# Performance work log

Hardware: AMD Instinct MI355X
Metric: run time of the kernel (lower is better)

The kernel has to match this reference:

```python
import jax, jax.numpy as jnp
import numpy as np

N_NODES = 50000
N_EDGES = 600000
D_EMB = 128
D_HID = 128
N_HEADS = 4
N_MABS = 7  # ISAB0(mab0,mab1), ISAB1(mab0,mab1), PMA, SAB, SAB
B, S = 16, 512
PROTO = 5


def setup_inputs() -> dict:
    key = jax.random.key(0)
    ks = jax.random.split(key, 24)
    nrm = lambda k, shape, s=0.05: jax.random.normal(k, shape, jnp.float32) * s
    node_embed = nrm(ks[0], (N_NODES + 1, D_EMB), 1.0).at[0].set(0.0)  # padding_idx=0
    return {
        'node_ids': jax.random.randint(ks[1], (B, S), 0, N_NODES),
        'edge_idx': jax.random.randint(ks[2], (2, N_EDGES), 0, N_NODES),
        'edge_attr': jax.random.normal(ks[3], (N_EDGES,), jnp.float32),
        'node_embed': node_embed,
        'lin_W': nrm(ks[4], (D_EMB, D_HID)), 'lin_b': jnp.zeros((D_HID,), jnp.float32),
        'gat_W': nrm(ks[5], (D_HID, D_HID)),
        'gat_att_src': nrm(ks[6], (D_HID,)), 'gat_att_dst': nrm(ks[7], (D_HID,)),
        'gat_bias': jnp.zeros((D_HID,), jnp.float32),
        'mab_Wq': nrm(ks[8], (N_MABS, D_HID, D_HID)), 'mab_bq': jnp.zeros((N_MABS, D_HID), jnp.float32),
        'mab_Wk': nrm(ks[9], (N_MABS, D_HID, D_HID)), 'mab_bk': jnp.zeros((N_MABS, D_HID), jnp.float32),
        'mab_Wv': nrm(ks[10], (N_MABS, D_HID, D_HID)), 'mab_bv': jnp.zeros((N_MABS, D_HID), jnp.float32),
        'mab_Wo': nrm(ks[11], (N_MABS, D_HID, D_HID)), 'mab_bo': jnp.zeros((N_MABS, D_HID), jnp.float32),
        'isab_I': nrm(ks[12], (2, 1, D_HID), 1.0),   # 2 ISAB blocks, num_inds=1
        'pma_S': nrm(ks[13], (1, D_HID), 1.0),       # num_outputs=1 seed
        'dec_W': nrm(ks[14], (D_HID, D_HID)), 'dec_b': jnp.zeros((D_HID,), jnp.float32),
        'prototypes': nrm(ks[15], (1, PROTO, D_HID), 1.0),
    }


def mab(Q, K, Wq, bq, Wk, bk, Wv, bv, Wo, bo):
    # Set-transformer MAB, ln=False; residual uses projected Q; scale by sqrt(full dim)
    D = Q.shape[-1]
    h, d = N_HEADS, D // N_HEADS
    Qp = Q @ Wq + bq
    Kp = K @ Wk + bk
    Vp = K @ Wv + bv
    sh = lambda x: x.reshape(x.shape[0], x.shape[1], h, d).transpose(0, 2, 1, 3)
    A = jax.nn.softmax(jnp.einsum('bhqd,bhkd->bhqk', sh(Qp), sh(Kp)) / np.sqrt(D).astype(np.float32))
    O = sh(Qp) + jnp.einsum('bhqk,bhkd->bhqd', A, sh(Vp))
    O = O.transpose(0, 2, 1, 3).reshape(Q.shape[0], Q.shape[1], D)
    return O + jax.nn.relu(O @ Wo + bo)


def reference(node_ids, edge_idx, edge_attr, node_embed, lin_W, lin_b, gat_W,
              gat_att_src, gat_att_dst, gat_bias, mab_Wq, mab_bq, mab_Wk, mab_bk,
              mab_Wv, mab_bv, mab_Wo, mab_bo, isab_I, pma_S, dec_W, dec_b, prototypes):
    # embed all nodes then linear
    x = node_embed[jnp.arange(N_NODES)] @ lin_W + lin_b          # [N, H]
    # GATConv (1 head, negative_slope=0.2, add_self_loops=True; edge_attr unused)
    loops = jnp.arange(N_NODES)
    src = jnp.concatenate([edge_idx[0], loops])
    dst = jnp.concatenate([edge_idx[1], loops])
    xw = x @ gat_W                                               # [N, H]
    a_s = xw @ gat_att_src                                       # [N]
    a_d = xw @ gat_att_dst
    e = jax.nn.leaky_relu(a_s[src] + a_d[dst], 0.2)              # [E+N]
    m = jax.ops.segment_max(e, dst, num_segments=N_NODES)
    ex = jnp.exp(e - m[dst])
    den = jax.ops.segment_sum(ex, dst, num_segments=N_NODES)
    coef = ex / den[dst]
    x = jax.ops.segment_sum(coef[:, None] * xw[src], dst, num_segments=N_NODES) + gat_bias
    # gather per-sample node sets
    X = x[node_ids]                                              # [B, S, H]
    b = X.shape[0]
    def mb(i, Q, K):
        return mab(Q, K, mab_Wq[i], mab_bq[i], mab_Wk[i], mab_bk[i],
                   mab_Wv[i], mab_bv[i], mab_Wo[i], mab_bo[i])
    # encoder: 2 ISAB blocks (num_inds=1)
    for i in range(2):
        Hb = mb(2 * i, jnp.broadcast_to(isab_I[i][None], (b, 1, D_HID)), X)
        X = mb(2 * i + 1, X, Hb)
    # decoder: PMA -> SAB -> SAB -> Linear
    X = mb(4, jnp.broadcast_to(pma_S[None], (b, 1, D_HID)), X)
    X = mb(5, X, X)
    X = mb(6, X, X)
    X = X @ dec_W + dec_b                                        # [B, 1, H]
    proto = jnp.broadcast_to(prototypes, (b, PROTO, D_HID))
    return jnp.concatenate([X, proto], axis=1)                   # [B, 6, H]
```

## Files before the change

kernel.cpp:

```cpp
#include <hip/hip_runtime.h>
#include <math.h>

#define N_NODES 50000
#define N_EDGES 600000
#define BATCH 16
#define SEQ 512
#define NROWS (BATCH*SEQ)
#define N_ITEMS (N_EDGES + N_NODES)

#define OFF_X      0L
#define OFF_ACC    1048576L
#define OFF_X2     2097152L
#define OFF_AS     3145728L
#define OFF_AD     3195728L
#define OFF_WC     3245728L
#define OFF_BC     3262112L
#define OFF_QP     3262240L
#define OFF_WKH    3262624L
#define OFF_CKH    3264160L
#define OFF_VAS    3264176L
#define OFF_VAD    3264304L
#define OFF_BFIN   3264432L
#define OFF_CSD    3264560L
#define OFF_VPOD   3264564L
#define OFF_PWH    3266612L
#define OFF_PWL    3307572L
#define OFF_MASK   3348532L
#define OFF_DEG    (OFF_MASK + 50000L)
#define OFF_FILL   (OFF_DEG + 8192L)
#define OFF_CNT    (OFF_FILL + 8192L)
#define ZERO_BYTES ((50000L + 8192L + 8192L + 4L) * 4L)
#define OFF_MAP    (OFF_CNT + 4L)
#define OFF_INV    (OFF_MAP + 50000L)
#define OFF_ROWPTR (OFF_INV + 8192L)
#define OFF_COL    (OFF_ROWPTR + 8194L)

typedef __attribute__((ext_vector_type(8))) short bf16x8;
typedef __attribute__((ext_vector_type(4))) float f32x4;
#define MFMA16(a,b,c) __builtin_amdgcn_mfma_f32_16x16x32_bf16(a,b,c,0,0,0)

__device__ __forceinline__ unsigned short f2bf_rne(float f) {
    unsigned int u = __float_as_uint(f);
    unsigned int r = u + 0x7FFFu + ((u >> 16) & 1u);
    return (unsigned short)(r >> 16);
}
__device__ __forceinline__ float bf2f(unsigned short h) {
    return __uint_as_float(((unsigned int)h) << 16);
}

__global__ __launch_bounds__(256) void prep_kernel(
    const float* __restrict__ lin_W, const float* __restrict__ lin_b,
    const float* __restrict__ gat_W,
    const float* __restrict__ mab_Wq, const float* __restrict__ mab_bq,
    const float* __restrict__ isab_I, const float* __restrict__ pma_S,
    float* __restrict__ Wc, float* __restrict__ bc, float* __restrict__ qp)
{
    int t = blockIdx.x * 256 + threadIdx.x;
    if (t < 16384) {
        int i = t >> 7, j = t & 127;
        float s = 0.f;
        for (int k = 0; k < 128; ++k) s += lin_W[i*128 + k] * gat_W[k*128 + j];
        Wc[t] = s;
    } else if (t < 16512) {
        int j = t - 16384;
        float s = 0.f;
        for (int k = 0; k < 128; ++k) s += lin_b[k] * gat_W[k*128 + j];
        bc[j] = s;
    } else if (t < 16896) {
        int u = t - 16512;
        int m = u >> 7, c = u & 127;
        int mi = m * 2;
        const float* vec = (m == 0) ? isab_I : (m == 1 ? isab_I + 128 : pma_S);
        float s = mab_bq[mi*128 + c];
        for (int k = 0; k < 128; ++k) s += vec[k] * mab_Wq[mi*16384 + k*128 + c];
        qp[u] = s;
    }
}

__global__ __launch_bounds__(256) void pack2_kernel(
    const float* __restrict__ Wc, const float* __restrict__ bc,
    const float* __restrict__ qp,
    const float* __restrict__ mab_Wq, const float* __restrict__ mab_Wo,
    const float* __restrict__ mab_Wk, const float* __restrict__ mab_bk,
    const float* __restrict__ att_src, const float* __restrict__ att_dst,
    const float* __restrict__ gat_bias,
    unsigned short* __restrict__ pWh, unsigned short* __restrict__ pWl,
    float* __restrict__ wkh, float* __restrict__ ckh,
    float* __restrict__ vas, float* __restrict__ vad,
    float* __restrict__ bfin, float* __restrict__ csd)
{
    int b = blockIdx.x, t = threadIdx.x;
    if (b < 320) {
        int tid = b*256 + t;
        int m = tid >> 14;
        int e = tid & 16383;
        int j = e & 7, l = (e>>3) & 63, ct = (e>>9) & 7, kc = e >> 12;
        int k = kc*32 + (l>>4)*8 + j;
        int c = ct*16 + (l & 15);
        const float* src;
        if (m == 0) src = Wc;
        else if (m == 1) src = mab_Wq + 1*16384;
        else if (m == 2) src = mab_Wo + 1*16384;
        else if (m == 3) src = mab_Wq + 3*16384;
        else src = mab_Wo + 3*16384;
        float v = src[k*128 + c];
        unsigned short h = f2bf_rne(v);
        pWh[tid] = h;
        pWl[tid] = f2bf_rne(v - bf2f(h));
    } else if (b == 320) {
        for (int it = 0; it < 6; ++it) {
            int u = it*256 + t;
            int m = u >> 9, h = (u >> 7) & 3, j = u & 127;
            const float* Wk = mab_Wk + (2*m)*16384 + j*128 + h*32;
            const float* q  = qp + m*128 + h*32;
            float s = 0.f;
            #pragma unroll
            for (int d = 0; d < 32; ++d) s += Wk[d] * q[d];
            wkh[u] = s;
        }
        if (t < 12) {
            int m = t >> 2, h = t & 3;
            const float* bk = mab_bk + (2*m)*128 + h*32;
            const float* q  = qp + m*128 + h*32;
            float s = 0.f;
            #pragma unroll
            for (int d = 0; d < 32; ++d) s += bk[d] * q[d];
            ckh[t] = s;
        }
    } else {
        if (t < 128) {
            float s = 0.f;
            for (int j = 0; j < 128; ++j) s += Wc[t*128 + j] * att_src[j];
            vas[t] = s;
            bfin[t] = bc[t] + gat_bias[t];
        } else {
            int k = t - 128;
            float s = 0.f;
            for (int j = 0; j < 128; ++j) s += Wc[k*128 + j] * att_dst[j];
            vad[k] = s;
        }
        if (t == 0) {
            float s = 0.f;
            for (int j = 0; j < 128; ++j) s += bc[j] * att_src[j];
            csd[0] = s;
        }
        if (t == 1) {
            float s = 0.f;
            for (int j = 0; j < 128; ++j) s += bc[j] * att_dst[j];
            csd[1] = s;
        }
    }
}

__device__ __forceinline__ void mfma_stage(
    const float (*Xs)[132], int arow, int ao, int lane,
    const unsigned short* __restrict__ pWh, const unsigned short* __restrict__ pWl,
    f32x4 acc[8])
{
    #pragma unroll
    for (int kc = 0; kc < 4; ++kc) {
        float4 fa = *(const float4*)&Xs[arow][kc*32 + ao];
        float4 fb = *(const float4*)&Xs[arow][kc*32 + ao + 4];
        float f[8] = {fa.x, fa.y, fa.z, fa.w, fb.x, fb.y, fb.z, fb.w};
        bf16x8 ah, al;
        #pragma unroll
        for (int j = 0; j < 8; ++j) {
            unsigned short h = f2bf_rne(f[j]);
            ah[j] = (short)h;
            al[j] = (short)f2bf_rne(f[j] - bf2f(h));
        }
        #pragma unroll
        for (int ct = 0; ct < 8; ++ct) {
            int fo = ((kc*8 + ct)*64 + lane)*8;
            bf16x8 bh = *(const bf16x8*)(pWh + fo);
            bf16x8 bl = *(const bf16x8*)(pWl + fo);
            acc[ct] = MFMA16(ah, bh, acc[ct]);
            acc[ct] = MFMA16(ah, bl, acc[ct]);
            acc[ct] = MFMA16(al, bh, acc[ct]);
        }
    }
}

__global__ __launch_bounds__(256) void mfma_lin_kernel(
    const float* __restrict__ Xin,
    const unsigned short* __restrict__ pWh, const unsigned short* __restrict__ pWl,
    const float* __restrict__ b1, float* __restrict__ out)
{
    __shared__ float Xs[64][132];
    int t = threadIdx.x;
    long row0 = (long)blockIdx.x * 64;
    #pragma unroll
    for (int i = 0; i < 32; ++i) {
        int idx = i*256 + t;
        int r = idx >> 7, k = idx & 127;
        Xs[r][k] = Xin[(row0 + r)*128 + k];
    }
    __syncthreads();
    int lane = t & 63, wv = t >> 6;
    int arow = wv*16 + (lane & 15), ao = (lane >> 4)*8;
    int crow0 = wv*16 + (lane >> 4)*4, ccol = lane & 15;
    f32x4 acc[8];
    #pragma unroll
    for (int ct = 0; ct < 8; ++ct) { acc[ct][0]=0.f; acc[ct][1]=0.f; acc[ct][2]=0.f; acc[ct][3]=0.f; }
    mfma_stage(Xs, arow, ao, lane, pWh, pWl, acc);
    #pragma unroll
    for (int ct = 0; ct < 8; ++ct) {
        int cc = ct*16 + ccol;
        float bb = b1[cc];
        #pragma unroll
        for (int i = 0; i < 4; ++i)
            out[(row0 + crow0 + i)*128 + cc] = acc[ct][i] + bb;
    }
}

__global__ __launch_bounds__(256) void mfma_odd_kernel(
    const float* __restrict__ Xin,
    const unsigned short* __restrict__ pQh, const unsigned short* __restrict__ pQl,
    const float* __restrict__ bq, const float* __restrict__ vpod,
    const unsigned short* __restrict__ pOh, const unsigned short* __restrict__ pOl,
    const float* __restrict__ bo, float* __restrict__ Xout)
{
    __shared__ float Xs[64][132];
    int t = threadIdx.x;
    long row0 = (long)blockIdx.x * 64;
    #pragma unroll
    for (int i = 0; i < 32; ++i) {
        int idx = i*256 + t;
        int r = idx >> 7, k = idx & 127;
        Xs[r][k] = Xin[(row0 + r)*128 + k];
    }
    __syncthreads();
    int lane = t & 63, wv = t >> 6;
    int arow = wv*16 + (lane & 15), ao = (lane >> 4)*8;
    int crow0 = wv*16 + (lane >> 4)*4, ccol = lane & 15;
    int bidx = (int)(row0 >> 9);
    f32x4 acc[8];
    #pragma unroll
    for (int ct = 0; ct < 8; ++ct) { acc[ct][0]=0.f; acc[ct][1]=0.f; acc[ct][2]=0.f; acc[ct][3]=0.f; }
    mfma_stage(Xs, arow, ao, lane, pQh, pQl, acc);
    #pragma unroll
    for (int ct = 0; ct < 8; ++ct) {
        int cc = ct*16 + ccol;
        float bb = bq[cc] + vpod[bidx*128 + cc];
        #pragma unroll
        for (int i = 0; i < 4; ++i) Xs[crow0 + i][cc] = acc[ct][i] + bb;
    }
    #pragma unroll
    for (int ct = 0; ct < 8; ++ct) { acc[ct][0]=0.f; acc[ct][1]=0.f; acc[ct][2]=0.f; acc[ct][3]=0.f; }
    mfma_stage(Xs, arow, ao, lane, pOh, pOl, acc);
    #pragma unroll
    for (int ct = 0; ct < 8; ++ct) {
        int cc = ct*16 + ccol;
        float bb = bo[cc];
        #pragma unroll
        for (int i = 0; i < 4; ++i) {
            float o1 = Xs[crow0 + i][cc];
            Xout[(row0 + crow0 + i)*128 + cc] = o1 + fmaxf(acc[ct][i] + bb, 0.f);
        }
    }
}

__global__ __launch_bounds__(256) void avec_kernel(
    const float* __restrict__ embed, const float* __restrict__ vas,
    const float* __restrict__ vad, const float* __restrict__ csd,
    const int* __restrict__ node_ids, int* __restrict__ mask,
    float* __restrict__ a_s, float* __restrict__ a_d)
{
    if (blockIdx.x < 32) {
        int idx = blockIdx.x*256 + threadIdx.x;
        mask[node_ids[idx]] = 1;
    }
    int w = threadIdx.x >> 6, lane = threadIdx.x & 63;
    long row = (long)blockIdx.x * 4 + w;
    const float* xr = embed + row*128 + lane*2;
    float x0 = xr[0], x1 = xr[1];
    float s = x0*vas[lane*2] + x1*vas[lane*2 + 1];
    float d = x0*vad[lane*2] + x1*vad[lane*2 + 1];
    #pragma unroll
    for (int off = 32; off > 0; off >>= 1) {
        s += __shfl_down(s, off);
        d += __shfl_down(d, off);
    }
    if (lane == 0) { a_s[row] = s + csd[0]; a_d[row] = d + csd[1]; }
}

__global__ __launch_bounds__(256) void assign_kernel(
    const int* __restrict__ mask, int* __restrict__ map,
    int* __restrict__ inv, int* __restrict__ counter)
{
    __shared__ int wbase[4];
    int i = blockIdx.x*256 + threadIdx.x;
    bool act = (i < N_NODES) && mask[i];
    unsigned long long m = __ballot(act);
    int lane = threadIdx.x & 63;
    int w = threadIdx.x >> 6;
    if (lane == 0) wbase[w] = __popcll(m);
    __syncthreads();
    if (threadIdx.x == 0) {
        int tot = wbase[0] + wbase[1] + wbase[2] + wbase[3];
        int base = atomicAdd(counter, tot);
        int r = base;
        #pragma unroll
        for (int j = 0; j < 4; ++j) { int cj = wbase[j]; wbase[j] = r; r += cj; }
    }
    __syncthreads();
    if (i < N_NODES) {
        int c = -1;
        if (act) {
            c = wbase[w] + __popcll(m & ((1ull << lane) - 1ull));
            inv[c] = i;
        }
        map[i] = c;
    }
}

__global__ __launch_bounds__(256) void pass1_kernel(
    const int* __restrict__ edge_idx, const int* __restrict__ map,
    int* __restrict__ deg)
{
    int i = blockIdx.x*256 + threadIdx.x;
    if (i >= N_ITEMS) return;
    int dd = (i < N_EDGES) ? edge_idx[N_EDGES + i] : i - N_EDGES;
    int c = map[dd];
    if (c >= 0) atomicAdd(&deg[c], 1);
}

__global__ __launch_bounds__(256) void scan_kernel(const int* __restrict__ deg,
                                                   int* __restrict__ rowptr)
{
    __shared__ int part[256];
    __shared__ int pref[256];
    int t = threadIdx.x;
    int base = t * 32;
    int s = 0;
    #pragma unroll
    for (int j = 0; j < 32; ++j) s += deg[base + j];
    part[t] = s;
    __syncthreads();
    if (t == 0) {
        int run = 0;
        for (int i = 0; i < 256; ++i) { pref[i] = run; run += part[i]; }
    }
    __syncthreads();
    int run = pref[t];
    #pragma unroll
    for (int j = 0; j < 32; ++j) { rowptr[base + j] = run; run += deg[base + j]; }
    if (t == 255) rowptr[8192] = run;
}

__global__ __launch_bounds__(256) void pass2_kernel(
    const int* __restrict__ edge_idx, const int* __restrict__ map,
    const int* __restrict__ rowptr, int* __restrict__ fill,
    int* __restrict__ colx)
{
    int i = blockIdx.x*256 + threadIdx.x;
    if (i >= N_ITEMS) return;
    int s, dd;
    if (i < N_EDGES) { s = edge_idx[i]; dd = edge_idx[N_EDGES + i]; }
    else             { s = dd = i - N_EDGES; }
    int c = map[dd];
    if (c < 0) return;
    int pos = rowptr[c] + atomicAdd(&fill[c], 1);
    colx[pos] = s;
}

__global__ __launch_bounds__(256) void agg_kernel(
    const int* __restrict__ rowptr, const int* __restrict__ colx,
    const int* __restrict__ inv, const int* __restrict__ cnt,
    const float* __restrict__ a_s, const float* __restrict__ a_d,
    const float* __restrict__ embed, float* __restrict__ acc)
{
    int c = blockIdx.x*4 + (threadIdx.x >> 6);
    int lane = threadIdx.x & 63;
    if (c >= *cnt) return;
    int dd = inv[c];
    float ad = a_d[dd];
    int beg = rowptr[c], end = rowptr[c + 1];
    float s0 = 0.f, s1 = 0.f, den = 0.f;
    for (int j = beg; j < end; ++j) {
        int s = colx[j];
        float e = a_s[s] + ad;
        e = (e > 0.f) ? e : 0.2f * e;
        float ex = __expf(e);
        den += ex;
        float2 v = *(const float2*)(embed + (long)s*128 + lane*2);
        s0 += ex * v.x;
        s1 += ex * v.y;
    }
    float inv_d = 1.f / den;
    float* o = acc + (long)c*128 + lane*2;
    o[0] = s0 * inv_d;
    o[1] = s1 * inv_d;
}

__global__ __launch_bounds__(256) void gather_kernel(
    const int* __restrict__ node_ids, const int* __restrict__ map,
    const float* __restrict__ X2, float* __restrict__ X)
{
    int w = threadIdx.x >> 6, lane = threadIdx.x & 63;
    int j = blockIdx.x*4 + w;
    int c = map[node_ids[j]];
    const float2 v = *(const float2*)(X2 + (long)c*128 + lane*2);
    *(float2*)(X + (long)j*128 + lane*2) = v;
}

__device__ __forceinline__ float matvec_qs(
    const float* __restrict__ W, const float* xs, float (*red)[128], int t)
{
    int c = t & 127, q = t >> 7;
    float acc = 0.f;
    #pragma unroll
    for (int j = 0; j < 32; ++j) {
        int k = q*32 + j;
        acc += xs[k] * W[k*128 + c];
    }
    red[q][c] = acc;
    __syncthreads();
    float s = 0.f;
    if (t < 128) s = red[0][t] + red[1][t] + red[2][t] + red[3][t];
    __syncthreads();
    return s;
}

__global__ __launch_bounds__(512) void attn_even_kernel(
    const float* __restrict__ X, const float* __restrict__ qp,
    const float* __restrict__ wkh, const float* __restrict__ ckh,
    const float* __restrict__ Wv, const float* __restrict__ bv,
    const float* __restrict__ Wo, const float* __restrict__ bo,
    const float* __restrict__ Wv1, const float* __restrict__ bv1,
    float* __restrict__ vpod)
{
    __shared__ float l_sm[4][512];
    __shared__ float part[4][4][128];
    __shared__ float wks[4][128];
    __shared__ float u_sm[4][128];
    __shared__ float red[4][128];
    __shared__ float red64[4][64];
    __shared__ float mx[4], dn[4];
    __shared__ float qs[128], Ovec[128], Hsm[128];
    int b = blockIdx.x, t = threadIdx.x;
    if (t < 128) qs[t] = qp[t];
    wks[t >> 7][t & 127] = wkh[t];
    __syncthreads();
    const float scale = 0.088388347648318447f;
    float ck0 = ckh[0], ck1 = ckh[1], ck2 = ckh[2], ck3 = ckh[3];
    {
        const float* xr = X + ((long)b*512 + t)*128;
        float l[4] = {0.f, 0.f, 0.f, 0.f};
        for (int d4 = 0; d4 < 128; d4 += 4) {
            float4 xv = *(const float4*)&xr[d4];
            #pragma unroll
            for (int h = 0; h < 4; ++h)
                l[h] += xv.x*wks[h][d4] + xv.y*wks[h][d4+1]
                      + xv.z*wks[h][d4+2] + xv.w*wks[h][d4+3];
        }
        l_sm[0][t] = (l[0] + ck0) * scale;
        l_sm[1][t] = (l[1] + ck1) * scale;
        l_sm[2][t] = (l[2] + ck2) * scale;
        l_sm[3][t] = (l[3] + ck3) * scale;
    }
    __syncthreads();
    if (t < 256) {
        int h = t >> 6, i = t & 63;
        float m = -1e30f;
        #pragma unroll
        for (int j = 0; j < 8; ++j) m = fmaxf(m, l_sm[h][i + 64*j]);
        red64[h][i] = m;
    }
    __syncthreads();
    if (t < 4) {
        float m = -1e30f;
        for (int i = 0; i < 64; ++i) m = fmaxf(m, red64[t][i]);
        mx[t] = m;
    }
    __syncthreads();
    #pragma unroll
    for (int h = 0; h < 4; ++h) l_sm[h][t] = __expf(l_sm[h][t] - mx[h]);
    __syncthreads();
    if (t < 256) {
        int h = t >> 6, i = t & 63;
        float ssum = 0.f;
        #pragma unroll
        for (int j = 0; j < 8; ++j) ssum += l_sm[h][i + 64*j];
        red64[h][i] = ssum;
    }
    __syncthreads();
    if (t < 4) {
        float sm = 0.f;
        for (int i = 0; i < 64; ++i) sm += red64[t][i];
        dn[t] = 1.f / sm;
    }
    __syncthreads();
    {
        int q4 = t >> 7, d = t & 127;
        float a0 = 0.f, a1 = 0.f, a2 = 0.f, a3 = 0.f;
        const float* xc = X + ((long)b*512 + q4*128)*128 + d;
        for (int kk = 0; kk < 128; ++kk) {
            float xv = xc[(long)kk*128];
            int k = q4*128 + kk;
            a0 += xv * l_sm[0][k];
            a1 += xv * l_sm[1][k];
            a2 += xv * l_sm[2][k];
            a3 += xv * l_sm[3][k];
        }
        part[q4][0][d] = a0; part[q4][1][d] = a1; part[q4][2][d] = a2; part[q4][3][d] = a3;
    }
    __syncthreads();
    {
        int h = t >> 7, d = t & 127;
        u_sm[h][d] = (part[0][h][d] + part[1][h][d] + part[2][h][d] + part[3][h][d]) * dn[h];
    }
    __syncthreads();
    {
        int q4 = t >> 7, c = t & 127, h = c >> 5;
        float a = 0.f;
        #pragma unroll
        for (int j = 0; j < 32; ++j) {
            int k = q4*32 + j;
            a += u_sm[h][k] * Wv[k*128 + c];
        }
        red[q4][c] = a;
    }
    __syncthreads();
    if (t < 128) Ovec[t] = qs[t] + red[0][t] + red[1][t] + red[2][t] + red[3][t] + bv[t];
    __syncthreads();
    float mv = matvec_qs(Wo, Ovec, red, t);
    if (t < 128) Hsm[t] = Ovec[t] + fmaxf(mv + bo[t], 0.f);
    __syncthreads();
    float mv2 = matvec_qs(Wv1, Hsm, red, t);
    if (t < 128) vpod[b*128 + t] = mv2 + bv1[t];
}

__global__ __launch_bounds__(512) void attn_pma_kernel(
    const float* __restrict__ X, const float* __restrict__ qp,
    const float* __restrict__ wkh, const float* __restrict__ ckh,
    const float* __restrict__ mab_Wq, const float* __restrict__ mab_bq,
    const float* __restrict__ mab_Wv, const float* __restrict__ mab_bv,
    const float* __restrict__ mab_Wo, const float* __restrict__ mab_bo,
    const float* __restrict__ dec_W, const float* __restrict__ dec_b,
    const float* __restrict__ protos, float* __restrict__ out)
{
    __shared__ float l_sm[4][512];
    __shared__ float part[4][4][128];
    __shared__ float wks[4][128];
    __shared__ float u_sm[4][128];
    __shared__ float red[4][128];
    __shared__ float red64[4][64];
    __shared__ float mx[4], dn[4];
    __shared__ float qs[128], Ovec[128], S1[128], S2[128];
    int b = blockIdx.x, t = threadIdx.x;
    if (t < 128) qs[t] = qp[t];
    wks[t >> 7][t & 127] = wkh[t];
    __syncthreads();
    const float scale = 0.088388347648318447f;
    float ck0 = ckh[0], ck1 = ckh[1], ck2 = ckh[2], ck3 = ckh[3];
    {
        const float* xr = X + ((long)b*512 + t)*128;
        float l[4] = {0.f, 0.f, 0.f, 0.f};
        for (int d4 = 0; d4 < 128; d4 += 4) {
            float4 xv = *(const float4*)&xr[d4];
            #pragma unroll
            for (int h = 0; h < 4; ++h)
                l[h] += xv.x*wks[h][d4] + xv.y*wks[h][d4+1]
                      + xv.z*wks[h][d4+2] + xv.w*wks[h][d4+3];
        }
        l_sm[0][t] = (l[0] + ck0) * scale;
        l_sm[1][t] = (l[1] + ck1) * scale;
        l_sm[2][t] = (l[2] + ck2) * scale;
        l_sm[3][t] = (l[3] + ck3) * scale;
    }
    __syncthreads();
    if (t < 256) {
        int h = t >> 6, i = t & 63;
        float m = -1e30f;
        #pragma unroll
        for (int j = 0; j < 8; ++j) m = fmaxf(m, l_sm[h][i + 64*j]);
        red64[h][i] = m;
    }
    __syncthreads();
    if (t < 4) {
        float m = -1e30f;
        for (int i = 0; i < 64; ++i) m = fmaxf(m, red64[t][i]);
        mx[t] = m;
    }
    __syncthreads();
    #pragma unroll
    for (int h = 0; h < 4; ++h) l_sm[h][t] = __expf(l_sm[h][t] - mx[h]);
    __syncthreads();
    if (t < 256) {
        int h = t >> 6, i = t & 63;
        float ssum = 0.f;
        #pragma unroll
        for (int j = 0; j < 8; ++j) ssum += l_sm[h][i + 64*j];
        red64[h][i] = ssum;
    }
    __syncthreads();
    if (t < 4) {
        float sm = 0.f;
        for (int i = 0; i < 64; ++i) sm += red64[t][i];
        dn[t] = 1.f / sm;
    }
    __syncthreads();
    {
        int q4 = t >> 7, d = t & 127;
        float a0 = 0.f, a1 = 0.f, a2 = 0.f, a3 = 0.f;
        const float* xc = X + ((long)b*512 + q4*128)*128 + d;
        for (int kk = 0; kk < 128; ++kk) {
            float xv = xc[(long)kk*128];
            int k = q4*128 + kk;
            a0 += xv * l_sm[0][k];
            a1 += xv * l_sm[1][k];
            a2 += xv * l_sm[2][k];
            a3 += xv * l_sm[3][k];
        }
        part[q4][0][d] = a0; part[q4][1][d] = a1; part[q4][2][d] = a2; part[q4][3][d] = a3;
    }
    __syncthreads();
    {
        int h = t >> 7, d = t & 127;
        u_sm[h][d] = (part[0][h][d] + part[1][h][d] + part[2][h][d] + part[3][h][d]) * dn[h];
    }
    __syncthreads();
    {
        int q4 = t >> 7, c = t & 127, h = c >> 5;
        float a = 0.f;
        #pragma unroll
        for (int j = 0; j < 32; ++j) {
            int k = q4*32 + j;
            a += u_sm[h][k] * (mab_Wv + 4*16384)[k*128 + c];
        }
        red[q4][c] = a;
    }
    __syncthreads();
    if (t < 128) Ovec[t] = qs[t] + red[0][t] + red[1][t] + red[2][t] + red[3][t]
                         + mab_bv[4*128 + t];
    __syncthreads();
    float mv = matvec_qs(mab_Wo + 4*16384, Ovec, red, t);
    if (t < 128) S1[t] = Ovec[t] + fmaxf(mv + mab_bo[4*128 + t], 0.f);
    __syncthreads();
    float q5 = matvec_qs(mab_Wq + 5*16384, S1, red, t);
    float v5 = matvec_qs(mab_Wv + 5*16384, S1, red, t);
    if (t < 128) S2[t] = q5 + mab_bq[5*128 + t] + v5 + mab_bv[5*128 + t];
    __syncthreads();
    float m5 = matvec_qs(mab_Wo + 5*16384, S2, red, t);
    if (t < 128) S1[t] = S2[t] + fmaxf(m5 + mab_bo[5*128 + t], 0.f);
    __syncthreads();
    float q6 = matvec_qs(mab_Wq + 6*16384, S1, red, t);
    float v6 = matvec_qs(mab_Wv + 6*16384, S1, red, t);
    if (t < 128) S2[t] = q6 + mab_bq[6*128 + t] + v6 + mab_bv[6*128 + t];
    __syncthreads();
    float m6 = matvec_qs(mab_Wo + 6*16384, S2, red, t);
    if (t < 128) S1[t] = S2[t] + fmaxf(m6 + mab_bo[6*128 + t], 0.f);
    __syncthreads();
    float y = matvec_qs(dec_W, S1, red, t);
    if (t < 128) out[b*768 + t] = y + dec_b[t];
    {
        int p = t >> 7, c = t & 127;
        out[b*768 + (1 + p)*128 + c] = protos[p*128 + c];
        if (t < 128) out[b*768 + 640 + t] = protos[512 + t];
    }
}

extern "C" void kernel_launch(void* const* d_in, const int* in_sizes, int n_in,
                              void* d_out, int out_size, void* d_ws, size_t ws_size,
                              hipStream_t stream)
{
    (void)in_sizes; (void)n_in; (void)out_size; (void)ws_size;
    const int*   node_ids  = (const int*)d_in[0];
    const int*   edge_idx  = (const int*)d_in[1];
    const float* node_embed= (const float*)d_in[3];
    const float* lin_W     = (const float*)d_in[4];
    const float* lin_b     = (const float*)d_in[5];
    const float* gat_W     = (const float*)d_in[6];
    const float* att_src   = (const float*)d_in[7];
    const float* att_dst   = (const float*)d_in[8];
    const float* gat_bias  = (const float*)d_in[9];
    const float* mab_Wq    = (const float*)d_in[10];
    const float* mab_bq    = (const float*)d_in[11];
    const float* mab_Wk    = (const float*)d_in[12];
    const float* mab_bk    = (const float*)d_in[13];
    const float* mab_Wv    = (const float*)d_in[14];
    const float* mab_bv    = (const float*)d_in[15];
    const float* mab_Wo    = (const float*)d_in[16];
    const float* mab_bo    = (const float*)d_in[17];
    const float* isab_I    = (const float*)d_in[18];
    const float* pma_S     = (const float*)d_in[19];
    const float* dec_W     = (const float*)d_in[20];
    const float* dec_b     = (const float*)d_in[21];
    const float* protos    = (const float*)d_in[22];

    float* ws    = (float*)d_ws;
    float* X     = ws + OFF_X;
    float* acc   = ws + OFF_ACC;
    float* X2    = ws + OFF_X2;
    float* a_s   = ws + OFF_AS;
    float* a_d   = ws + OFF_AD;
    float* Wc    = ws + OFF_WC;
    float* bc    = ws + OFF_BC;
    float* qp    = ws + OFF_QP;
    float* wkh   = ws + OFF_WKH;
    float* ckh   = ws + OFF_CKH;
    float* vas   = ws + OFF_VAS;
    float* vad   = ws + OFF_VAD;
    float* bfin  = ws + OFF_BFIN;
    float* csd   = ws + OFF_CSD;
    float* vpod  = ws + OFF_VPOD;
    unsigned short* pWh = (unsigned short*)(ws + OFF_PWH);
    unsigned short* pWl = (unsigned short*)(ws + OFF_PWL);
    int*   mask  = (int*)(ws + OFF_MASK);
    int*   deg   = (int*)(ws + OFF_DEG);
    int*   fill  = (int*)(ws + OFF_FILL);
    int*   cnt   = (int*)(ws + OFF_CNT);
    int*   map   = (int*)(ws + OFF_MAP);
    int*   inv   = (int*)(ws + OFF_INV);
    int*   rowp  = (int*)(ws + OFF_ROWPTR);
    int*   colx  = (int*)(ws + OFF_COL);
    float* out   = (float*)d_out;

    hipMemsetAsync(ws + OFF_MASK, 0, ZERO_BYTES, stream);

    prep_kernel<<<66, 256, 0, stream>>>(lin_W, lin_b, gat_W, mab_Wq, mab_bq, isab_I, pma_S,
                                        Wc, bc, qp);
    pack2_kernel<<<322, 256, 0, stream>>>(Wc, bc, qp, mab_Wq, mab_Wo, mab_Wk, mab_bk,
                                          att_src, att_dst, gat_bias,
                                          pWh, pWl, wkh, ckh, vas, vad, bfin, csd);
    avec_kernel<<<N_NODES/4, 256, 0, stream>>>(node_embed, vas, vad, csd, node_ids, mask,
                                               a_s, a_d);
    assign_kernel<<<(N_NODES + 255)/256, 256, 0, stream>>>(mask, map, inv, cnt);
    pass1_kernel<<<(N_ITEMS + 255)/256, 256, 0, stream>>>(edge_idx, map, deg);
    scan_kernel<<<1, 256, 0, stream>>>(deg, rowp);
    pass2_kernel<<<(N_ITEMS + 255)/256, 256, 0, stream>>>(edge_idx, map, rowp, fill, colx);
    agg_kernel<<<NROWS/4, 256, 0, stream>>>(rowp, colx, inv, cnt, a_s, a_d, node_embed, acc);
    mfma_lin_kernel<<<NROWS/64, 256, 0, stream>>>(acc, pWh, pWl, bfin, X2);
    gather_kernel<<<NROWS/4, 256, 0, stream>>>(node_ids, map, X2, X);

    for (int i = 0; i < 2; ++i) {
        int o = 2*i + 1;
        attn_even_kernel<<<16, 512, 0, stream>>>(X, qp + i*128, wkh + i*512, ckh + i*4,
                                                 mab_Wv + (2*i)*16384, mab_bv + (2*i)*128,
                                                 mab_Wo + (2*i)*16384, mab_bo + (2*i)*128,
                                                 mab_Wv + o*16384, mab_bv + o*128,
                                                 vpod);
        int mq = 1 + 2*i;
        int mo = 2 + 2*i;
        mfma_odd_kernel<<<NROWS/64, 256, 0, stream>>>(X,
                                                      pWh + mq*16384, pWl + mq*16384,
                                                      mab_bq + o*128, vpod,
                                                      pWh + mo*16384, pWl + mo*16384,
                                                      mab_bo + o*128, X);
    }
    attn_pma_kernel<<<16, 512, 0, stream>>>(X, qp + 256, wkh + 1024, ckh + 8,
                                            mab_Wq, mab_bq, mab_Wv, mab_bv, mab_Wo, mab_bo,
                                            dec_W, dec_b, protos, out);
}
```

Before: 297.7 us.

## Split single-query attention into chunked partial-sum kernel plus combine kernel

The per-batch attention pooling, which ran on only 16 blocks, is split into two kernels. The first runs 128 blocks, each computing exp-scores and partial weighted sums over a 64-row chunk. The second combines the 8 chunk partials and runs the small matvec tail. The softmax drops its max subtraction, which trades numerical safety for parallelism and adds one extra launch and a global round-trip per attention stage.

```diff
diff --git a/kernel.cpp b/kernel.cpp
--- a/kernel.cpp
+++ b/kernel.cpp
@@ -23,9 +23,11 @@
 #define OFF_BFIN   3264432L
 #define OFF_CSD    3264560L
 #define OFF_VPOD   3264564L
-#define OFF_PWH    3266612L
-#define OFF_PWL    3307572L
-#define OFF_MASK   3348532L
+#define OFF_UP     3266612L
+#define OFF_SP     3332148L
+#define OFF_PWH    3332660L
+#define OFF_PWL    3373620L
+#define OFF_MASK   3414580L
 #define OFF_DEG    (OFF_MASK + 50000L)
 #define OFF_FILL   (OFF_DEG + 8192L)
 #define OFF_CNT    (OFF_FILL + 8192L)
@@ -404,6 +406,52 @@
     *(float2*)(X + (long)j*128 + lane*2) = v;
 }
 
+__global__ __launch_bounds__(256) void attn_partA_kernel(
+    const float* __restrict__ X, const float* __restrict__ wkh,
+    const float* __restrict__ ckh, float* __restrict__ up, float* __restrict__ sp)
+{
+    __shared__ float wks[4][128];
+    __shared__ float esm[4][64];
+    int b = blockIdx.x >> 3, chunk = blockIdx.x & 7;
+    int t = threadIdx.x;
+    #pragma unroll
+    for (int i = 0; i < 2; ++i) {
+        int u = i*256 + t;
+        wks[u >> 7][u & 127] = wkh[u];
+    }
+    __syncthreads();
+    const float scale = 0.088388347648318447f;
+    int wv = t >> 6, lane = t & 63;
+    {
+        const float* xr = X + ((long)b*512 + chunk*64 + lane)*128;
+        float l = 0.f;
+        for (int d4 = 0; d4 < 128; d4 += 4) {
+            float4 xv = *(const float4*)&xr[d4];
+            l += xv.x*wks[wv][d4] + xv.y*wks[wv][d4+1]
+               + xv.z*wks[wv][d4+2] + xv.w*wks[wv][d4+3];
+        }
+        float e = __expf((l + ckh[wv]) * scale);
+        esm[wv][lane] = e;
+        float s = e;
+        #pragma unroll
+        for (int off = 32; off > 0; off >>= 1) s += __shfl_down(s, off);
+        if (lane == 0) sp[(b*8 + chunk)*4 + wv] = s;
+    }
+    __syncthreads();
+    {
+        int hh = t >> 7, d = t & 127;
+        float a0 = 0.f, a1 = 0.f;
+        const float* xc = X + ((long)b*512 + chunk*64)*128 + d;
+        for (int k = 0; k < 64; ++k) {
+            float xv = xc[(long)k*128];
+            a0 += esm[2*hh][k] * xv;
+            a1 += esm[2*hh + 1][k] * xv;
+        }
+        up[((b*8 + chunk)*4 + 2*hh)*128 + d] = a0;
+        up[((b*8 + chunk)*4 + 2*hh + 1)*128 + d] = a1;
+    }
+}
+
 __device__ __forceinline__ float matvec_qs(
     const float* __restrict__ W, const float* xs, float (*red)[128], int t)
 {
@@ -422,93 +470,28 @@
     return s;
 }
 
-__global__ __launch_bounds__(512) void attn_even_kernel(
-    const float* __restrict__ X, const float* __restrict__ qp,
-    const float* __restrict__ wkh, const float* __restrict__ ckh,
+__global__ __launch_bounds__(512) void attn_evenB_kernel(
+    const float* __restrict__ up, const float* __restrict__ sp,
+    const float* __restrict__ qp,
     const float* __restrict__ Wv, const float* __restrict__ bv,
     const float* __restrict__ Wo, const float* __restrict__ bo,
     const float* __restrict__ Wv1, const float* __restrict__ bv1,
     float* __restrict__ vpod)
 {
-    __shared__ float l_sm[4][512];
-    __shared__ float part[4][4][128];
-    __shared__ float wks[4][128];
     __shared__ float u_sm[4][128];
     __shared__ float red[4][128];
-    __shared__ float red64[4][64];
-    __shared__ float mx[4], dn[4];
     __shared__ float qs[128], Ovec[128], Hsm[128];
     int b = blockIdx.x, t = threadIdx.x;
     if (t < 128) qs[t] = qp[t];
-    wks[t >> 7][t & 127] = wkh[t];
-    __syncthreads();
-    const float scale = 0.088388347648318447f;
-    float ck0 = ckh[0], ck1 = ckh[1], ck2 = ckh[2], ck3 = ckh[3];
-    {
-        const float* xr = X + ((long)b*512 + t)*128;
-        float l[4] = {0.f, 0.f, 0.f, 0.f};
-        for (int d4 = 0; d4 < 128; d4 += 4) {
-            float4 xv = *(const float4*)&xr[d4];
-            #pragma unroll
-            for (int h = 0; h < 4; ++h)
-                l[h] += xv.x*wks[h][d4] + xv.y*wks[h][d4+1]
-                      + xv.z*wks[h][d4+2] + xv.w*wks[h][d4+3];
-        }
-        l_sm[0][t] = (l[0] + ck0) * scale;
-        l_sm[1][t] = (l[1] + ck1) * scale;
-        l_sm[2][t] = (l[2] + ck2) * scale;
-        l_sm[3][t] = (l[3] + ck3) * scale;
-    }
-    __syncthreads();
-    if (t < 256) {
-        int h = t >> 6, i = t & 63;
-        float m = -1e30f;
-        #pragma unroll
-        for (int j = 0; j < 8; ++j) m = fmaxf(m, l_sm[h][i + 64*j]);
-        red64[h][i] = m;
-    }
-    __syncthreads();
-    if (t < 4) {
-        float m = -1e30f;
-        for (int i = 0; i < 64; ++i) m = fmaxf(m, red64[t][i]);
-        mx[t] = m;
-    }
-    __syncthreads();
-    #pragma unroll
-    for (int h = 0; h < 4; ++h) l_sm[h][t] = __expf(l_sm[h][t] - mx[h]);
-    __syncthreads();
-    if (t < 256) {
-        int h = t >> 6, i = t & 63;
-        float ssum = 0.f;
-        #pragma unroll
-        for (int j = 0; j < 8; ++j) ssum += l_sm[h][i + 64*j];
-        red64[h][i] = ssum;
-    }
-    __syncthreads();
-    if (t < 4) {
-        float sm = 0.f;
-        for (int i = 0; i < 64; ++i) sm += red64[t][i];
-        dn[t] = 1.f / sm;
-    }
-    __syncthreads();
-    {
-        int q4 = t >> 7, d = t & 127;
-        float a0 = 0.f, a1 = 0.f, a2 = 0.f, a3 = 0.f;
-        const float* xc = X + ((long)b*512 + q4*128)*128 + d;
-        for (int kk = 0; kk < 128; ++kk) {
-            float xv = xc[(long)kk*128];
-            int k = q4*128 + kk;
-            a0 += xv * l_sm[0][k];
-            a1 += xv * l_sm[1][k];
-            a2 += xv * l_sm[2][k];
-            a3 += xv * l_sm[3][k];
-        }
-        part[q4][0][d] = a0; part[q4][1][d] = a1; part[q4][2][d] = a2; part[q4][3][d] = a3;
-    }
-    __syncthreads();
     {
         int h = t >> 7, d = t & 127;
-        u_sm[h][d] = (part[0][h][d] + part[1][h][d] + part[2][h][d] + part[3][h][d]) * dn[h];
+        float s = 0.f, dn = 0.f;
+        #pragma unroll
+        for (int c = 0; c < 8; ++c) {
+            s  += up[((b*8 + c)*4 + h)*128 + d];
+            dn += sp[(b*8 + c)*4 + h];
+        }
+        u_sm[h][d] = s / dn;
     }
     __syncthreads();
     {
@@ -531,94 +514,29 @@
     if (t < 128) vpod[b*128 + t] = mv2 + bv1[t];
 }
 
-__global__ __launch_bounds__(512) void attn_pma_kernel(
-    const float* __restrict__ X, const float* __restrict__ qp,
-    const float* __restrict__ wkh, const float* __restrict__ ckh,
+__global__ __launch_bounds__(512) void attn_pmaB_kernel(
+    const float* __restrict__ up, const float* __restrict__ sp,
+    const float* __restrict__ qp,
     const float* __restrict__ mab_Wq, const float* __restrict__ mab_bq,
     const float* __restrict__ mab_Wv, const float* __restrict__ mab_bv,
     const float* __restrict__ mab_Wo, const float* __restrict__ mab_bo,
     const float* __restrict__ dec_W, const float* __restrict__ dec_b,
     const float* __restrict__ protos, float* __restrict__ out)
 {
-    __shared__ float l_sm[4][512];
-    __shared__ float part[4][4][128];
-    __shared__ float wks[4][128];
     __shared__ float u_sm[4][128];
     __shared__ float red[4][128];
-    __shared__ float red64[4][64];
-    __shared__ float mx[4], dn[4];
     __shared__ float qs[128], Ovec[128], S1[128], S2[128];
     int b = blockIdx.x, t = threadIdx.x;
     if (t < 128) qs[t] = qp[t];
-    wks[t >> 7][t & 127] = wkh[t];
-    __syncthreads();
-    const float scale = 0.088388347648318447f;
-    float ck0 = ckh[0], ck1 = ckh[1], ck2 = ckh[2], ck3 = ckh[3];
-    {
-        const float* xr = X + ((long)b*512 + t)*128;
-        float l[4] = {0.f, 0.f, 0.f, 0.f};
-        for (int d4 = 0; d4 < 128; d4 += 4) {
-            float4 xv = *(const float4*)&xr[d4];
-            #pragma unroll
-            for (int h = 0; h < 4; ++h)
-                l[h] += xv.x*wks[h][d4] + xv.y*wks[h][d4+1]
-                      + xv.z*wks[h][d4+2] + xv.w*wks[h][d4+3];
-        }
-        l_sm[0][t] = (l[0] + ck0) * scale;
-        l_sm[1][t] = (l[1] + ck1) * scale;
-        l_sm[2][t] = (l[2] + ck2) * scale;
-        l_sm[3][t] = (l[3] + ck3) * scale;
-    }
-    __syncthreads();
-    if (t < 256) {
-        int h = t >> 6, i = t & 63;
-        float m = -1e30f;
-        #pragma unroll
-        for (int j = 0; j < 8; ++j) m = fmaxf(m, l_sm[h][i + 64*j]);
-        red64[h][i] = m;
-    }
-    __syncthreads();
-    if (t < 4) {
-        float m = -1e30f;
-        for (int i = 0; i < 64; ++i) m = fmaxf(m, red64[t][i]);
-        mx[t] = m;
-    }
-    __syncthreads();
-    #pragma unroll
-    for (int h = 0; h < 4; ++h) l_sm[h][t] = __expf(l_sm[h][t] - mx[h]);
-    __syncthreads();
-    if (t < 256) {
-        int h = t >> 6, i = t & 63;
-        float ssum = 0.f;
-        #pragma unroll
-        for (int j = 0; j < 8; ++j) ssum += l_sm[h][i + 64*j];
-        red64[h][i] = ssum;
-    }
-    __syncthreads();
-    if (t < 4) {
-        float sm = 0.f;
-        for (int i = 0; i < 64; ++i) sm += red64[t][i];
-        dn[t] = 1.f / sm;
-    }
-    __syncthreads();
-    {
-        int q4 = t >> 7, d = t & 127;
-        float a0 = 0.f, a1 = 0.f, a2 = 0.f, a3 = 0.f;
-        const float* xc = X + ((long)b*512 + q4*128)*128 + d;
-        for (int kk = 0; kk < 128; ++kk) {
-            float xv = xc[(long)kk*128];
-            int k = q4*128 + kk;
-            a0 += xv * l_sm[0][k];
-            a1 += xv * l_sm[1][k];
-            a2 += xv * l_sm[2][k];
-            a3 += xv * l_sm[3][k];
-        }
-        part[q4][0][d] = a0; part[q4][1][d] = a1; part[q4][2][d] = a2; part[q4][3][d] = a3;
-    }
-    __syncthreads();
     {
         int h = t >> 7, d = t & 127;
-        u_sm[h][d] = (part[0][h][d] + part[1][h][d] + part[2][h][d] + part[3][h][d]) * dn[h];
+        float s = 0.f, dn = 0.f;
+        #pragma unroll
+        for (int c = 0; c < 8; ++c) {
+            s  += up[((b*8 + c)*4 + h)*128 + d];
+            dn += sp[(b*8 + c)*4 + h];
+        }
+        u_sm[h][d] = s / dn;
     }
     __syncthreads();
     {
@@ -705,6 +623,8 @@
     float* bfin  = ws + OFF_BFIN;
     float* csd   = ws + OFF_CSD;
     float* vpod  = ws + OFF_VPOD;
+    float* up    = ws + OFF_UP;
+    float* sp    = ws + OFF_SP;
     unsigned short* pWh = (unsigned short*)(ws + OFF_PWH);
     unsigned short* pWl = (unsigned short*)(ws + OFF_PWL);
     int*   mask  = (int*)(ws + OFF_MASK);
@@ -736,11 +656,12 @@
 
     for (int i = 0; i < 2; ++i) {
         int o = 2*i + 1;
-        attn_even_kernel<<<16, 512, 0, stream>>>(X, qp + i*128, wkh + i*512, ckh + i*4,
-                                                 mab_Wv + (2*i)*16384, mab_bv + (2*i)*128,
-                                                 mab_Wo + (2*i)*16384, mab_bo + (2*i)*128,
-                                                 mab_Wv + o*16384, mab_bv + o*128,
-                                                 vpod);
+        attn_partA_kernel<<<128, 256, 0, stream>>>(X, wkh + i*512, ckh + i*4, up, sp);
+        attn_evenB_kernel<<<16, 512, 0, stream>>>(up, sp, qp + i*128,
+                                                  mab_Wv + (2*i)*16384, mab_bv + (2*i)*128,
+                                                  mab_Wo + (2*i)*16384, mab_bo + (2*i)*128,
+                                                  mab_Wv + o*16384, mab_bv + o*128,
+                                                  vpod);
         int mq = 1 + 2*i;
         int mo = 2 + 2*i;
         mfma_odd_kernel<<<NROWS/64, 256, 0, stream>>>(X,
@@ -749,7 +670,8 @@
                                                       pWh + mo*16384, pWl + mo*16384,
                                                       mab_bo + o*128, X);
     }
-    attn_pma_kernel<<<16, 512, 0, stream>>>(X, qp + 256, wkh + 1024, ckh + 8,
-                                            mab_Wq, mab_bq, mab_Wv, mab_bv, mab_Wo, mab_bo,
-                                            dec_W, dec_b, protos, out);
-}
+    attn_partA_kernel<<<128, 256, 0, stream>>>(X, wkh + 1024, ckh + 8, up, sp);
+    attn_pmaB_kernel<<<16, 512, 0, stream>>>(up, sp, qp + 256,
+                                             mab_Wq, mab_bq, mab_Wv, mab_bv, mab_Wo, mab_bo,
+                                             dec_W, dec_b, protos, out);
+}
```

New measurement: 302.6 us. Within noise of the previous version (+1.6%).
